# Kernel optimization log

Hardware: AMD Instinct MI355X
Metric: run time of the kernel (lower is better)

Reference implementation:

```python
import jax, jax.numpy as jnp
import numpy as np

E_INF = 1.5  # long-term modulus
E_MOD = 1.0  # Maxwell spring modulus
ETA = 2.0    # dashpot viscosity


def setup_inputs() -> dict:
    key = jax.random.key(0)
    k1, k2 = jax.random.split(key)
    B, T = 4096, 8192
    eps = jax.random.normal(k1, (B, T, 1), dtype=jnp.float32)          # strain history
    dt = jax.random.uniform(k2, (B, T, 1), dtype=jnp.float32)          # timestep sizes (>0)
    return {"eps": eps, "dt": dt}


def reference(eps, dt):
    # eps, dt: [B, T, 1]. Scan over time with internal variable gamma (state), gamma0 = 0.
    # Per step (matches MaxwellRNNCell.call):
    #   sig_n   = E_inf*eps_n + E*(eps_n - gamma_N)
    #   gamma_n = gamma_N + dt*(E/eta)*(eps_n - gamma_N)
    k = E_MOD / ETA
    eps_t = jnp.swapaxes(eps, 0, 1)  # [T, B, 1]
    dt_t = jnp.swapaxes(dt, 0, 1)    # [T, B, 1]

    def step(gamma, xs):
        e, d = xs
        diff = e - gamma
        sig = E_INF * e + E_MOD * diff
        gamma_new = gamma + d * k * diff
        return gamma_new, sig

    gamma0 = jnp.zeros((eps.shape[0], 1), dtype=eps.dtype)
    _, sig = jax.lax.scan(step, gamma0, (eps_t, dt_t))
    return jnp.swapaxes(sig, 0, 1)  # [B, T, 1]
```

## Files before the change

### kernel.cpp

```cpp
#include <hip/hip_runtime.h>


constexpr int   T_LEN   = 8192;
constexpr int   THREADS = 256;
constexpr int   V       = 8;
constexpr int   TILE    = THREADS * V;
constexpr int   NTILES  = T_LEN / TILE;
constexpr int   NWAVES  = THREADS / 64;
constexpr float KCOEF   = 0.5f;

__global__ __launch_bounds__(THREADS) void maxwell_scan_kernel(
    const float* __restrict__ eps, const float* __restrict__ dtv,
    float* __restrict__ out)
{
    const size_t row = (size_t)blockIdx.x * T_LEN;
    const float* e_row = eps + row;
    const float* d_row = dtv + row;
    float*       o_row = out + row;

    __shared__ float wA[NWAVES];
    __shared__ float wB[NWAVES];

    const int lane = threadIdx.x & 63;
    const int wid  = threadIdx.x >> 6;

    float gamma = 0.0f;

    for (int t = 0; t < NTILES; ++t) {
        const int base = t * TILE + threadIdx.x * V;

        float4 e0 = *(const float4*)(e_row + base);
        float4 e1 = *(const float4*)(e_row + base + 4);
        float4 d0 = *(const float4*)(d_row + base);
        float4 d1 = *(const float4*)(d_row + base + 4);
        float ev[V] = {e0.x, e0.y, e0.z, e0.w, e1.x, e1.y, e1.z, e1.w};
        float hv[V] = {d0.x * KCOEF, d0.y * KCOEF, d0.z * KCOEF, d0.w * KCOEF,
                       d1.x * KCOEF, d1.y * KCOEF, d1.z * KCOEF, d1.w * KCOEF};

        float A = 1.0f, Bc = 0.0f;
        #pragma unroll
        for (int j = 0; j < V; ++j) {
            float a = 1.0f - hv[j];
            Bc = a * Bc + hv[j] * ev[j];
            A  = a * A;
        }

        float sa = A, sb = Bc;
        #pragma unroll
        for (int off = 1; off < 64; off <<= 1) {
            float pa = __shfl_up(sa, off, 64);
            float pb = __shfl_up(sb, off, 64);
            if (lane >= off) {
                sb = sa * pb + sb;
                sa = sa * pa;
            }
        }
        if (lane == 63) { wA[wid] = sa; wB[wid] = sb; }
        __syncthreads();

        float ea = __shfl_up(sa, 1, 64);
        float eb = __shfl_up(sb, 1, 64);
        if (lane == 0) { ea = 1.0f; eb = 0.0f; }

        float pfa = 1.0f, pfb = 0.0f;
        float ta  = 1.0f, tb  = 0.0f;
        #pragma unroll
        for (int w = 0; w < NWAVES; ++w) {
            float a = wA[w], bb = wB[w];
            if (w < wid) { pfb = a * pfb + bb; pfa = a * pfa; }
            tb = a * tb + bb;
            ta = a * ta;
        }

        float xa = ea * pfa;
        float xb = ea * pfb + eb;
        float g  = xa * gamma + xb;

        float sg[V];
        #pragma unroll
        for (int j = 0; j < V; ++j) {
            sg[j] = 2.5f * ev[j] - g;
            g = g + hv[j] * (ev[j] - g);
        }
        *(float4*)(o_row + base)     = make_float4(sg[0], sg[1], sg[2], sg[3]);
        *(float4*)(o_row + base + 4) = make_float4(sg[4], sg[5], sg[6], sg[7]);

        gamma = ta * gamma + tb;
        __syncthreads();
    }
}

extern "C" void kernel_launch(void* const* d_in, const int* in_sizes, int n_in,
                              void* d_out, int out_size, void* d_ws, size_t ws_size,
                              hipStream_t stream) {
    const float* eps = (const float*)d_in[0];
    const float* dtv = (const float*)d_in[1];
    float* out = (float*)d_out;
    const int B = in_sizes[0] / T_LEN;
    maxwell_scan_kernel<<<B, THREADS, 0, stream>>>(eps, dtv, out);
}
```

Baseline: 307.4 us.

## Cover whole row in one tile with 512 threads and nontemporal stores

Each block now processes the full 8192-element row in a single pass, using 512 threads with 16 elements each. This removes the tile loop, the carried gamma state and the second barrier per tile. The cross-wave prefix drops the unused A product because the initial gamma is zero. Output is written with nontemporal vector stores to avoid cache pollution, and launch bounds request higher occupancy. Per-thread register pressure rises and the serial per-thread recurrence is longer.

```diff
diff --git a/kernel.cpp b/kernel.cpp
--- a/kernel.cpp
+++ b/kernel.cpp
@@ -2,14 +2,14 @@
 
 
 constexpr int   T_LEN   = 8192;
-constexpr int   THREADS = 256;
-constexpr int   V       = 8;
-constexpr int   TILE    = THREADS * V;
-constexpr int   NTILES  = T_LEN / TILE;
+constexpr int   THREADS = 512;
+constexpr int   V       = 16;
 constexpr int   NWAVES  = THREADS / 64;
 constexpr float KCOEF   = 0.5f;
 
-__global__ __launch_bounds__(THREADS) void maxwell_scan_kernel(
+typedef float f32x4 __attribute__((ext_vector_type(4)));
+
+__global__ __launch_bounds__(THREADS, 8) void maxwell_scan_kernel(
     const float* __restrict__ eps, const float* __restrict__ dtv,
     float* __restrict__ out)
 {
@@ -23,70 +23,66 @@
 
     const int lane = threadIdx.x & 63;
     const int wid  = threadIdx.x >> 6;
+    const int base = threadIdx.x * V;
 
-    float gamma = 0.0f;
+    f32x4 e0 = *(const f32x4*)(e_row + base);
+    f32x4 e1 = *(const f32x4*)(e_row + base + 4);
+    f32x4 e2 = *(const f32x4*)(e_row + base + 8);
+    f32x4 e3 = *(const f32x4*)(e_row + base + 12);
+    f32x4 d0 = *(const f32x4*)(d_row + base);
+    f32x4 d1 = *(const f32x4*)(d_row + base + 4);
+    f32x4 d2 = *(const f32x4*)(d_row + base + 8);
+    f32x4 d3 = *(const f32x4*)(d_row + base + 12);
 
-    for (int t = 0; t < NTILES; ++t) {
-        const int base = t * TILE + threadIdx.x * V;
+    float ev[V] = {e0.x, e0.y, e0.z, e0.w, e1.x, e1.y, e1.z, e1.w,
+                   e2.x, e2.y, e2.z, e2.w, e3.x, e3.y, e3.z, e3.w};
+    float hv[V] = {d0.x * KCOEF, d0.y * KCOEF, d0.z * KCOEF, d0.w * KCOEF,
+                   d1.x * KCOEF, d1.y * KCOEF, d1.z * KCOEF, d1.w * KCOEF,
+                   d2.x * KCOEF, d2.y * KCOEF, d2.z * KCOEF, d2.w * KCOEF,
+                   d3.x * KCOEF, d3.y * KCOEF, d3.z * KCOEF, d3.w * KCOEF};
 
-        float4 e0 = *(const float4*)(e_row + base);
-        float4 e1 = *(const float4*)(e_row + base + 4);
-        float4 d0 = *(const float4*)(d_row + base);
-        float4 d1 = *(const float4*)(d_row + base + 4);
-        float ev[V] = {e0.x, e0.y, e0.z, e0.w, e1.x, e1.y, e1.z, e1.w};
-        float hv[V] = {d0.x * KCOEF, d0.y * KCOEF, d0.z * KCOEF, d0.w * KCOEF,
-                       d1.x * KCOEF, d1.y * KCOEF, d1.z * KCOEF, d1.w * KCOEF};
+    float A = 1.0f, Bc = 0.0f;
+    #pragma unroll
+    for (int j = 0; j < V; ++j) {
+        float a = 1.0f - hv[j];
+        Bc = a * Bc + hv[j] * ev[j];
+        A  = a * A;
+    }
 
-        float A = 1.0f, Bc = 0.0f;
+    float sa = A, sb = Bc;
+    #pragma unroll
+    for (int off = 1; off < 64; off <<= 1) {
+        float pa = __shfl_up(sa, off, 64);
+        float pb = __shfl_up(sb, off, 64);
+        if (lane >= off) {
+            sb = sa * pb + sb;
+            sa = sa * pa;
+        }
+    }
+    if (lane == 63) { wA[wid] = sa; wB[wid] = sb; }
+    __syncthreads();
+
+    float ea = __shfl_up(sa, 1, 64);
+    float eb = __shfl_up(sb, 1, 64);
+    if (lane == 0) { ea = 1.0f; eb = 0.0f; }
+
+    float pfb = 0.0f;
+    for (int w = 0; w < wid; ++w) {
+        pfb = wA[w] * pfb + wB[w];
+    }
+
+    float g = ea * pfb + eb;
+
+    #pragma unroll
+    for (int q = 0; q < V / 4; ++q) {
+        f32x4 s;
         #pragma unroll
-        for (int j = 0; j < V; ++j) {
-            float a = 1.0f - hv[j];
-            Bc = a * Bc + hv[j] * ev[j];
-            A  = a * A;
+        for (int j = 0; j < 4; ++j) {
+            const int idx = q * 4 + j;
+            s[j] = 2.5f * ev[idx] - g;
+            g = g + hv[idx] * (ev[idx] - g);
         }
-
-        float sa = A, sb = Bc;
-        #pragma unroll
-        for (int off = 1; off < 64; off <<= 1) {
-            float pa = __shfl_up(sa, off, 64);
-            float pb = __shfl_up(sb, off, 64);
-            if (lane >= off) {
-                sb = sa * pb + sb;
-                sa = sa * pa;
-            }
-        }
-        if (lane == 63) { wA[wid] = sa; wB[wid] = sb; }
-        __syncthreads();
-
-        float ea = __shfl_up(sa, 1, 64);
-        float eb = __shfl_up(sb, 1, 64);
-        if (lane == 0) { ea = 1.0f; eb = 0.0f; }
-
-        float pfa = 1.0f, pfb = 0.0f;
-        float ta  = 1.0f, tb  = 0.0f;
-        #pragma unroll
-        for (int w = 0; w < NWAVES; ++w) {
-            float a = wA[w], bb = wB[w];
-            if (w < wid) { pfb = a * pfb + bb; pfa = a * pfa; }
-            tb = a * tb + bb;
-            ta = a * ta;
-        }
-
-        float xa = ea * pfa;
-        float xb = ea * pfb + eb;
-        float g  = xa * gamma + xb;
-
-        float sg[V];
-        #pragma unroll
-        for (int j = 0; j < V; ++j) {
-            sg[j] = 2.5f * ev[j] - g;
-            g = g + hv[j] * (ev[j] - g);
-        }
-        *(float4*)(o_row + base)     = make_float4(sg[0], sg[1], sg[2], sg[3]);
-        *(float4*)(o_row + base + 4) = make_float4(sg[4], sg[5], sg[6], sg[7]);
-
-        gamma = ta * gamma + tb;
-        __syncthreads();
+        __builtin_nontemporal_store(s, (f32x4*)(o_row + base + q * 4));
     }
 }
 
```

After: 468.9 us. 52.5% more time.
